# Optimization experiments

Hardware: AMD Instinct MI355X
Metric: run time of the kernel (lower is better)

Reference implementation:

```python
import jax, jax.numpy as jnp
import numpy as np

B, S, D, H, L = 16, 1024, 128, 8, 3
DFF = 4 * D  # 512
DH = D // H  # 16
NUM_CLASSES = 6


def layernorm(x, g, b, eps):
    mu = jnp.mean(x, axis=-1, keepdims=True)
    var = jnp.mean(jnp.square(x - mu), axis=-1, keepdims=True)
    return g * (x - mu) / jnp.sqrt(var + eps) + b


def setup_inputs() -> dict:
    key = jax.random.key(0)
    ks = jax.random.split(key, 16)
    sc = 0.05
    inp = {
        'x': jax.random.normal(ks[0], (B, S, D), dtype=jnp.float32),
        'Wq': jax.random.normal(ks[1], (L, D, D), dtype=jnp.float32) * sc,
        'bq': jnp.zeros((L, D), dtype=jnp.float32),
        'Wk': jax.random.normal(ks[2], (L, D, D), dtype=jnp.float32) * sc,
        'bk': jnp.zeros((L, D), dtype=jnp.float32),
        'Wv': jax.random.normal(ks[3], (L, D, D), dtype=jnp.float32) * sc,
        'bv': jnp.zeros((L, D), dtype=jnp.float32),
        'ln1_g': jnp.ones((L, D), dtype=jnp.float32),
        'ln1_b': jnp.zeros((L, D), dtype=jnp.float32),
        'W1': jax.random.normal(ks[4], (L, D, DFF), dtype=jnp.float32) * sc,
        'b1': jnp.zeros((L, DFF), dtype=jnp.float32),
        'W2': jax.random.normal(ks[5], (L, DFF, D), dtype=jnp.float32) * sc,
        'b2': jnp.zeros((L, D), dtype=jnp.float32),
        'ln2_g': jnp.ones((L, D), dtype=jnp.float32),
        'ln2_b': jnp.zeros((L, D), dtype=jnp.float32),
        'Wout': jax.random.normal(ks[6], (D, NUM_CLASSES), dtype=jnp.float32) * sc,
        'bout': jnp.zeros((NUM_CLASSES,), dtype=jnp.float32),
    }
    return inp


def reference(x, Wq, bq, Wk, bk, Wv, bv, ln1_g, ln1_b, W1, b1, W2, b2, ln2_g, ln2_b, Wout, bout):
    scale = 1.0 / jnp.sqrt(jnp.float32(DH))
    for l in range(L):
        # Q/K/V projections with ReLU activation (as in source Dense(..., relu))
        q = jax.nn.relu(jnp.einsum('bsd,de->bse', x, Wq[l]) + bq[l])
        k = jax.nn.relu(jnp.einsum('bsd,de->bse', x, Wk[l]) + bk[l])
        v = jax.nn.relu(jnp.einsum('bsd,de->bse', x, Wv[l]) + bv[l])
        # split-heads (tf.split axis=-1 / concat axis=0 == reshape to heads)
        qh = q.reshape(B, S, H, DH)
        kh = k.reshape(B, S, H, DH)
        vh = v.reshape(B, S, H, DH)
        scores = jnp.einsum('bqhd,bkhd->bhqk', qh, kh) * scale  # [B,H,S,S]
        attn = jax.nn.softmax(scores, axis=-1)
        o = jnp.einsum('bhqk,bkhd->bqhd', attn, vh).reshape(B, S, D)
        x = layernorm(o + x, ln1_g[l], ln1_b[l], 1e-8)
        # pointwise FFN (Conv1D kernel_size=1 == dense over last dim)
        h = jax.nn.relu(jnp.einsum('bsd,df->bsf', x, W1[l]) + b1[l])
        f = jnp.einsum('bsf,fd->bsd', h, W2[l]) + b2[l]
        x = layernorm(f + x, ln2_g[l], ln2_b[l], 1e-6)
    return jnp.einsum('bsd,dc->bsc', x, Wout) + bout
```

## Files before the change

kernel.cpp:

```cpp
#include <hip/hip_runtime.h>
#include <math.h>

#define Bq 16
#define Sq 1024
#define Dq 128
#define Hq 8
#define DHq 16
#define DFFq 512
#define Lq 3
#define NCLS 6
#define NROWS (Bq * Sq)
#define NX ((size_t)NROWS * Dq)

#define QSCL 0.36067376022224085f

typedef __attribute__((ext_vector_type(8))) short    bf16x8;
typedef __attribute__((ext_vector_type(4))) float    f32x4;
typedef __attribute__((ext_vector_type(4))) _Float16 f16x4;
typedef __attribute__((ext_vector_type(8))) _Float16 f16x8;
typedef __attribute__((ext_vector_type(2))) _Float16 f16x2;

__device__ inline ushort f32_to_bf16(float f) {
    union { float f; unsigned u; } v; v.f = f;
    unsigned r = v.u + 0x7fffu + ((v.u >> 16) & 1u);
    return (ushort)(r >> 16);
}

__device__ __forceinline__ float exp2_raw(float x) {
    float r;
    asm("v_exp_f32 %0, %1" : "=v"(r) : "v"(x));
    return r;
}

__device__ __forceinline__ float rcp_fast(float x) {
    float r;
    asm("v_rcp_f32 %0, %1" : "=v"(r) : "v"(x));
    return r;
}

__device__ __forceinline__ f16x2 pkrtz(float a, float b) {
    return __builtin_bit_cast(f16x2, __builtin_amdgcn_cvt_pkrtz(a, b));
}

__global__ __launch_bounds__(256) void prep_kernel(
    const float* __restrict__ Wqp, const float* __restrict__ Wkp,
    const float* __restrict__ Wvp, const float* __restrict__ W1p,
    const float* __restrict__ W2p, const float* __restrict__ xp,
    ushort* __restrict__ wbf, ushort* __restrict__ xbf)
{
    const int gid = blockIdx.x * 256 + threadIdx.x;
    if (gid < 147456) {
        const int w   = gid / 49152;
        const int rem = gid - w * 49152;
        const int l   = rem >> 14;
        const int idx = rem & 16383;
        const int k   = idx >> 7;
        const int n   = idx & 127;
        const float* src = (w == 0) ? Wqp : (w == 1) ? Wkp : Wvp;
        const float scl = (w == 0) ? QSCL : 1.0f;
        wbf[(size_t)(w * 3 + l) * 16384 + n * 128 + k] =
            f32_to_bf16(src[(size_t)l * 16384 + k * 128 + n] * scl);
    } else if (gid < 344064) {
        const int g   = gid - 147456;
        const int l   = g >> 16;
        const int idx = g & 65535;
        const int k   = idx >> 9;
        const int n   = idx & 511;
        wbf[147456 + (size_t)l * 65536 + n * 128 + k] =
            f32_to_bf16(W1p[(size_t)l * 65536 + k * 512 + n]);
    } else if (gid < 540672) {
        const int g   = gid - 344064;
        const int l   = g >> 16;
        const int idx = g & 65535;
        const int k   = idx >> 7;
        const int n   = idx & 127;
        wbf[344064 + (size_t)l * 65536 + n * 512 + k] =
            f32_to_bf16(W2p[(size_t)l * 65536 + k * 128 + n]);
    } else {
        const int g = gid - 540672;
        xbf[g] = f32_to_bf16(xp[g]);
    }
}

__global__ __launch_bounds__(256) void gemm_qkv(
    const ushort* __restrict__ A,
    const ushort* __restrict__ wq, const ushort* __restrict__ wk,
    const ushort* __restrict__ wv,
    const float* __restrict__ bqp, const float* __restrict__ bkp,
    const float* __restrict__ bvp,
    _Float16* __restrict__ qo, _Float16* __restrict__ ko,
    _Float16* __restrict__ vo)
{
    __shared__ ushort As[64 * 40];
    __shared__ ushort Bs[128 * 40];

    const int sel  = blockIdx.y;
    const ushort* Bt   = (sel == 0) ? wq : (sel == 1) ? wk : wv;
    const float*  bias = (sel == 0) ? bqp : (sel == 1) ? bkp : bvp;
    const float   bscl = (sel == 0) ? QSCL : 1.0f;

    const int tid  = threadIdx.x;
    const int row0 = blockIdx.x * 64;
    const int wave = tid >> 6;
    const int lane = tid & 63;
    const int quad = lane >> 4;
    const int m16  = lane & 15;
    const int wm   = wave >> 1;
    const int wn   = wave & 1;

    const int sar = tid >> 2;
    const int sac = (tid & 3) * 8;

    f32x4 acc[2][4];
    #pragma unroll
    for (int i = 0; i < 2; ++i)
        #pragma unroll
        for (int j = 0; j < 4; ++j) acc[i][j] = (f32x4)0.f;

    const int r1 = tid >> 2, r2 = r1 + 64;

    bf16x8 av  = *(const bf16x8*)(A  + (size_t)(row0 + sar) * 128 + sac);
    bf16x8 bv1 = *(const bf16x8*)(Bt + (size_t)r1 * 128 + sac);
    bf16x8 bv2 = *(const bf16x8*)(Bt + (size_t)r2 * 128 + sac);

    for (int k0 = 0; k0 < 128; k0 += 32) {
        __syncthreads();
        *(bf16x8*)&As[sar * 40 + sac] = av;
        *(bf16x8*)&Bs[r1 * 40 + sac]  = bv1;
        *(bf16x8*)&Bs[r2 * 40 + sac]  = bv2;
        __syncthreads();

        if (k0 < 96) {
            av  = *(const bf16x8*)(A  + (size_t)(row0 + sar) * 128 + k0 + 32 + sac);
            bv1 = *(const bf16x8*)(Bt + (size_t)r1 * 128 + k0 + 32 + sac);
            bv2 = *(const bf16x8*)(Bt + (size_t)r2 * 128 + k0 + 32 + sac);
        }

        bf16x8 af[2], bf[4];
        #pragma unroll
        for (int i = 0; i < 2; ++i)
            af[i] = *(const bf16x8*)&As[(32 * wm + 16 * i + m16) * 40 + quad * 8];
        #pragma unroll
        for (int j = 0; j < 4; ++j)
            bf[j] = *(const bf16x8*)&Bs[(64 * wn + 16 * j + m16) * 40 + quad * 8];
        #pragma unroll
        for (int i = 0; i < 2; ++i)
            #pragma unroll
            for (int j = 0; j < 4; ++j)
                acc[i][j] = __builtin_amdgcn_mfma_f32_16x16x32_bf16(af[i], bf[j], acc[i][j], 0, 0, 0);
    }

    #pragma unroll
    for (int i = 0; i < 2; ++i) {
        #pragma unroll
        for (int j = 0; j < 4; ++j) {
            const int col = 64 * wn + 16 * j + m16;
            const float bb = bias[col] * bscl;
            const int hh = col >> 4, dh = col & 15;
            #pragma unroll
            for (int r = 0; r < 4; ++r) {
                float val = fmaxf(acc[i][j][r] + bb, 0.f);
                const int gr = row0 + 32 * wm + 16 * i + quad * 4 + r;
                const int b = gr >> 10, s = gr & 1023;
                if (sel == 2) {
                    vo[(((size_t)b * Hq + hh) * DHq + dh) * Sq + s] = (_Float16)val;
                } else {
                    _Float16* outp = (sel == 0) ? qo : ko;
                    outp[(((size_t)b * Hq + hh) * Sq + s) * DHq + dh] = (_Float16)val;
                }
            }
        }
    }
}

__global__ __launch_bounds__(256, 3) void gemm_ffn_fused(
    const _Float16* __restrict__ o, const float* __restrict__ resid,
    const float* __restrict__ g1, const float* __restrict__ beta1,
    const ushort* __restrict__ W1t, const float* __restrict__ bias1,
    const ushort* __restrict__ W2t, const float* __restrict__ bias2,
    const float* __restrict__ g2, const float* __restrict__ beta2,
    float* __restrict__ xb,
    const ushort* __restrict__ wqn, const ushort* __restrict__ wkn,
    const ushort* __restrict__ wvn,
    const float* __restrict__ bqn, const float* __restrict__ bkn,
    const float* __restrict__ bvn,
    _Float16* __restrict__ qo, _Float16* __restrict__ ko,
    _Float16* __restrict__ vo, int do_next,
    const float* __restrict__ Wout, const float* __restrict__ bout,
    float* __restrict__ out, int last)
{
    __shared__ __align__(16) char smem[44544];
    ushort*    Af   = (ushort*)smem;
    ushort*    Hcc  = (ushort*)(smem + 8704);
    ushort*    Bs   = (ushort*)(smem + 17408);
    float*     wo_s = (float*)(smem + 17408);
    _Float16*  vals = (_Float16*)(smem + 35840);
    float*     mus  = (float*)(smem + 44288);
    float*     rsds = (float*)(smem + 44416);

    const int tid  = threadIdx.x;
    const int row0 = blockIdx.x * 32;
    const int wave = tid >> 6;
    const int lane = tid & 63;
    const int quad = lane >> 4;
    const int m16  = lane & 15;
    const int wm   = wave >> 1;
    const int wn   = wave & 1;
    const int sac  = (tid & 3) * 8;
    const int r1   = tid >> 2, r2 = r1 + 64;

    const int ca = lane * 2;
    const float2 gg  = *(const float2*)(g1 + ca);
    const float2 bt1 = *(const float2*)(beta1 + ca);
    f16x2  ovv[8];
    float2 rvv[8];
    #pragma unroll
    for (int it = 0; it < 8; ++it) {
        const size_t base = (size_t)(row0 + wave * 8 + it) * Dq;
        ovv[it] = *(const f16x2*)(o + base + ca);
        rvv[it] = *(const float2*)(resid + base + ca);
    }
    #pragma unroll
    for (int it = 0; it < 8; ++it) {
        const int rr = wave * 8 + it;
        const float v0 = (float)ovv[it][0] + rvv[it].x;
        const float v1 = (float)ovv[it][1] + rvv[it].y;

        float s = v0 + v1;
        #pragma unroll
        for (int off = 32; off > 0; off >>= 1) s += __shfl_xor(s, off, 64);
        const float mu = s * (1.f / 128.f);
        const float d0 = v0 - mu, d1 = v1 - mu;
        float vs = d0 * d0 + d1 * d1;
        #pragma unroll
        for (int off = 32; off > 0; off >>= 1) vs += __shfl_xor(vs, off, 64);
        const float rstd = rsqrtf(vs * (1.f / 128.f) + 1e-8f);

        const float rv0 = gg.x * d0 * rstd + bt1.x;
        const float rv1 = gg.y * d1 * rstd + bt1.y;
        ushort2 ab; ab.x = f32_to_bf16(rv0); ab.y = f32_to_bf16(rv1);
        *(ushort2*)&Af[rr * 136 + ca] = ab;
        f16x2 vv; vv[0] = (_Float16)rv0; vv[1] = (_Float16)rv1;
        *(f16x2*)&vals[rr * 132 + ca] = vv;
    }

    f32x4 acc[4], acc2[4];
    #pragma unroll
    for (int j = 0; j < 4; ++j) { acc[j] = (f32x4)0.f; acc2[j] = (f32x4)0.f; }

    bf16x8 w11 = *(const bf16x8*)(W1t + (size_t)r1 * 128 + sac);
    bf16x8 w12 = *(const bf16x8*)(W1t + (size_t)r1 * 128 + 32 + sac);
    bf16x8 w21 = *(const bf16x8*)(W1t + (size_t)r2 * 128 + sac);
    bf16x8 w22 = *(const bf16x8*)(W1t + (size_t)r2 * 128 + 32 + sac);

    #pragma unroll
    for (int t = 0; t < 16; ++t) {
        const int cc   = t >> 2;
        const int ph   = (t >> 1) & 1;
        const int half = t & 1;

        __syncthreads();
        *(bf16x8*)&Bs[r1 * 72 + sac]      = w11;
        *(bf16x8*)&Bs[r1 * 72 + 32 + sac] = w12;
        *(bf16x8*)&Bs[r2 * 72 + sac]      = w21;
        *(bf16x8*)&Bs[r2 * 72 + 32 + sac] = w22;
        __syncthreads();

        if (t < 15) {
            const int tn  = t + 1;
            const int nc  = tn >> 2, np = (tn >> 1) & 1, nh = tn & 1;
            if (np == 0) {
                const ushort* p = W1t + (size_t)(nc * 128) * 128 + nh * 64;
                w11 = *(const bf16x8*)(p + (size_t)r1 * 128 + sac);
                w12 = *(const bf16x8*)(p + (size_t)r1 * 128 + 32 + sac);
                w21 = *(const bf16x8*)(p + (size_t)r2 * 128 + sac);
                w22 = *(const bf16x8*)(p + (size_t)r2 * 128 + 32 + sac);
            } else {
                const ushort* p = W2t + nc * 128 + nh * 64;
                w11 = *(const bf16x8*)(p + (size_t)r1 * 512 + sac);
                w12 = *(const bf16x8*)(p + (size_t)r1 * 512 + 32 + sac);
                w21 = *(const bf16x8*)(p + (size_t)r2 * 512 + sac);
                w22 = *(const bf16x8*)(p + (size_t)r2 * 512 + 32 + sac);
            }
        } else if (do_next) {
            w11 = *(const bf16x8*)(wqn + (size_t)r1 * 128 + sac);
            w12 = *(const bf16x8*)(wqn + (size_t)r1 * 128 + 32 + sac);
            w21 = *(const bf16x8*)(wqn + (size_t)r2 * 128 + sac);
            w22 = *(const bf16x8*)(wqn + (size_t)r2 * 128 + 32 + sac);
        }

        const ushort* Asrc = ph ? Hcc : Af;
        #pragma unroll
        for (int hh = 0; hh < 2; ++hh) {
            const int kk = half * 64 + hh * 32;
            const bf16x8 af = *(const bf16x8*)&Asrc[(16 * wm + m16) * 136 + kk + quad * 8];
            bf16x8 bf[4];
            #pragma unroll
            for (int j = 0; j < 4; ++j)
                bf[j] = *(const bf16x8*)&Bs[(64 * wn + 16 * j + m16) * 72 + hh * 32 + quad * 8];
            if (ph == 0) {
                #pragma unroll
                for (int j = 0; j < 4; ++j)
                    acc[j] = __builtin_amdgcn_mfma_f32_16x16x32_bf16(af, bf[j], acc[j], 0, 0, 0);
            } else {
                #pragma unroll
                for (int j = 0; j < 4; ++j)
                    acc2[j] = __builtin_amdgcn_mfma_f32_16x16x32_bf16(af, bf[j], acc2[j], 0, 0, 0);
            }
        }

        if (ph == 0 && half == 1) {
            #pragma unroll
            for (int j = 0; j < 4; ++j) {
                const int col_l = 64 * wn + 16 * j + m16;
                const float bb = bias1[cc * 128 + col_l];
                #pragma unroll
                for (int r = 0; r < 4; ++r) {
                    const int row = 16 * wm + quad * 4 + r;
                    Hcc[row * 136 + col_l] = f32_to_bf16(fmaxf(acc[j][r] + bb, 0.f));
                }
                acc[j] = (f32x4)0.f;
            }
        }
    }

    __syncthreads();

    float vreg[4][4];
    #pragma unroll
    for (int j = 0; j < 4; ++j) {
        const int col = 64 * wn + 16 * j + m16;
        const float bb = bias2[col];
        #pragma unroll
        for (int r = 0; r < 4; ++r) {
            const int row = 16 * wm + quad * 4 + r;
            float v = acc2[j][r] + bb + (float)vals[row * 132 + col];
            vreg[j][r] = v;
            vals[row * 132 + col] = (_Float16)v;
        }
    }
    if (last) {
        #pragma unroll
        for (int i = 0; i < 3; ++i) wo_s[tid + i * 256] = Wout[tid + i * 256];
    }
    __syncthreads();

    {
        const int row = tid >> 3;
        const int c0  = (tid & 7) * 16;
        float s = 0.f, s2 = 0.f;
        #pragma unroll
        for (int u = 0; u < 4; ++u) {
            const f16x4 xv = *(const f16x4*)&vals[row * 132 + c0 + u * 4];
            #pragma unroll
            for (int e = 0; e < 4; ++e) {
                const float x = (float)xv[e];
                s += x; s2 = fmaf(x, x, s2);
            }
        }
        s  += __shfl_xor(s, 1, 64);  s  += __shfl_xor(s, 2, 64);  s  += __shfl_xor(s, 4, 64);
        s2 += __shfl_xor(s2, 1, 64); s2 += __shfl_xor(s2, 2, 64); s2 += __shfl_xor(s2, 4, 64);
        if ((tid & 7) == 0) {
            const float mu  = s * (1.f / 128.f);
            const float var = s2 * (1.f / 128.f) - mu * mu;
            mus[row]  = mu;
            rsds[row] = rsqrtf(var + 1e-6f);
        }
    }
    __syncthreads();

    if (!last) {
        #pragma unroll
        for (int j = 0; j < 4; ++j) {
            const int col = 64 * wn + 16 * j + m16;
            #pragma unroll
            for (int r = 0; r < 4; ++r) {
                const int row = 16 * wm + quad * 4 + r;
                const float rn = g2[col] * (vreg[j][r] - mus[row]) * rsds[row] + beta2[col];
                xb[(size_t)(row0 + row) * Dq + col] = rn;
                Af[row * 136 + col] = f32_to_bf16(rn);
            }
        }

        if (do_next) {
            f32x4 qacc[4];
            #pragma unroll
            for (int st = 0; st < 6; ++st) {
                const int sel  = st >> 1;
                const int half = st & 1;
                if (half == 0) {
                    #pragma unroll
                    for (int j = 0; j < 4; ++j) qacc[j] = (f32x4)0.f;
                }

                __syncthreads();
                *(bf16x8*)&Bs[r1 * 72 + sac]      = w11;
                *(bf16x8*)&Bs[r1 * 72 + 32 + sac] = w12;
                *(bf16x8*)&Bs[r2 * 72 + sac]      = w21;
                *(bf16x8*)&Bs[r2 * 72 + 32 + sac] = w22;
                __syncthreads();

                if (st < 5) {
                    const int sel2 = (st + 1) >> 1;
                    const int k02  = ((st + 1) & 1) * 64;
                    const ushort* Bt2 = (sel2 == 0) ? wqn : (sel2 == 1) ? wkn : wvn;
                    w11 = *(const bf16x8*)(Bt2 + (size_t)r1 * 128 + k02 + sac);
                    w12 = *(const bf16x8*)(Bt2 + (size_t)r1 * 128 + k02 + 32 + sac);
                    w21 = *(const bf16x8*)(Bt2 + (size_t)r2 * 128 + k02 + sac);
                    w22 = *(const bf16x8*)(Bt2 + (size_t)r2 * 128 + k02 + 32 + sac);
                }

                const int k0 = half * 64;
                #pragma unroll
                for (int hh = 0; hh < 2; ++hh) {
                    const int kk = k0 + hh * 32;
                    const bf16x8 af = *(const bf16x8*)&Af[(16 * wm + m16) * 136 + kk + quad * 8];
                    bf16x8 bf[4];
                    #pragma unroll
                    for (int j = 0; j < 4; ++j)
                        bf[j] = *(const bf16x8*)&Bs[(64 * wn + 16 * j + m16) * 72 + hh * 32 + quad * 8];
                    #pragma unroll
                    for (int j = 0; j < 4; ++j)
                        qacc[j] = __builtin_amdgcn_mfma_f32_16x16x32_bf16(af, bf[j], qacc[j], 0, 0, 0);
                }

                if (half) {
                    const float* bias = (sel == 0) ? bqn : (sel == 1) ? bkn : bvn;
                    const float  bscl = (sel == 0) ? QSCL : 1.0f;
                    #pragma unroll
                    for (int j = 0; j < 4; ++j) {
                        const int col = 64 * wn + 16 * j + m16;
                        const float bb = bias[col] * bscl;
                        const int hh = col >> 4, dh = col & 15;
                        #pragma unroll
                        for (int r = 0; r < 4; ++r) {
                            float val = fmaxf(qacc[j][r] + bb, 0.f);
                            const int gr = row0 + 16 * wm + quad * 4 + r;
                            const int b = gr >> 10, s = gr & 1023;
                            if (sel == 2) {
                                vo[(((size_t)b * Hq + hh) * DHq + dh) * Sq + s] = (_Float16)val;
                            } else {
                                _Float16* outp = (sel == 0) ? qo : ko;
                                outp[(((size_t)b * Hq + hh) * Sq + s) * DHq + dh] = (_Float16)val;
                            }
                        }
                    }
                }
            }
        }
    } else {
        #pragma unroll
        for (int j = 0; j < 4; ++j) {
            const int col = 64 * wn + 16 * j + m16;
            #pragma unroll
            for (int r = 0; r < 4; ++r) {
                const int row = 16 * wm + quad * 4 + r;
                vals[row * 132 + col] =
                    (_Float16)(g2[col] * (vreg[j][r] - mus[row]) * rsds[row] + beta2[col]);
            }
        }
        __syncthreads();
        if (tid < 32 * NCLS) {
            const int row = tid / NCLS;
            const int c   = tid - row * NCLS;
            float a = bout[c];
            #pragma unroll 8
            for (int kk = 0; kk < Dq; ++kk)
                a = fmaf((float)vals[row * 132 + kk], wo_s[kk * NCLS + c], a);
            out[(size_t)(row0 + row) * NCLS + c] = a;
        }
    }
}

__global__ __launch_bounds__(256) void attn_mfma(
    const _Float16* __restrict__ q, const _Float16* __restrict__ k,
    const _Float16* __restrict__ vt, _Float16* __restrict__ o)
{
    __shared__ _Float16 Ks[256 * 20];
    __shared__ _Float16 Vs[16 * 264];

    const int bh   = blockIdx.x;
    const int qc   = blockIdx.y;
    const int b    = bh >> 3;
    const int h    = bh & 7;
    const int tid  = threadIdx.x;
    const int wave = tid >> 6;
    const int lane = tid & 63;
    const int quad = lane >> 4;
    const int m16  = lane & 15;
    const int q0   = qc * 128 + wave * 32;

    const f16x4 qf0 = *(const f16x4*)(q + (((size_t)bh * Sq) + q0 + m16) * DHq + quad * 4);
    const f16x4 qf1 = *(const f16x4*)(q + (((size_t)bh * Sq) + q0 + 16 + m16) * DHq + quad * 4);

    const _Float16* kg  = k  + (size_t)bh * Sq * DHq;
    const _Float16* vtg = vt + (size_t)bh * DHq * Sq;

    f32x4 oacc0 = (f32x4)0.f, oacc1 = (f32x4)0.f;
    f32x4 dacc0 = (f32x4)0.f, dacc1 = (f32x4)0.f;

    f16x4 onesf;
    onesf[0] = (_Float16)1.f; onesf[1] = (_Float16)1.f;
    onesf[2] = (_Float16)1.f; onesf[3] = (_Float16)1.f;

    const int krow = tid;
    const int vrow = tid >> 4;
    const int vcol = (tid & 15) * 16;

    f16x8 ka  = *(const f16x8*)(kg + (size_t)krow * DHq);
    f16x8 kb8 = *(const f16x8*)(kg + (size_t)krow * DHq + 8);
    f16x8 va  = *(const f16x8*)(vtg + (size_t)vrow * Sq + vcol);
    f16x8 vb  = *(const f16x8*)(vtg + (size_t)vrow * Sq + vcol + 8);

    for (int kb = 0; kb < 4; ++kb) {
        __syncthreads();
        *(f16x8*)&Ks[krow * 20 + 0] = ka;
        *(f16x8*)&Ks[krow * 20 + 8] = kb8;
        *(f16x8*)&Vs[vrow * 264 + vcol + 0] = va;
        *(f16x8*)&Vs[vrow * 264 + vcol + 8] = vb;
        __syncthreads();

        if (kb < 3) {
            const _Float16* kp = kg  + ((size_t)(kb + 1) * 256 + krow) * DHq;
            const _Float16* vp = vtg + (size_t)vrow * Sq + (kb + 1) * 256 + vcol;
            ka  = *(const f16x8*)(kp);
            kb8 = *(const f16x8*)(kp + 8);
            va  = *(const f16x8*)(vp);
            vb  = *(const f16x8*)(vp + 8);
        }

        __builtin_amdgcn_s_setprio(1);
        #pragma unroll 4
        for (int kt = 0; kt < 16; ++kt) {
            const f16x4 kf = *(const f16x4*)&Ks[(kt * 16 + m16) * 20 + quad * 4];
            const f16x4 vf = *(const f16x4*)&Vs[m16 * 264 + kt * 16 + quad * 4];

            f32x4 st0 = __builtin_amdgcn_mfma_f32_16x16x16f16(kf, qf0, (f32x4)0.f, 0, 0, 0);
            f32x4 st1 = __builtin_amdgcn_mfma_f32_16x16x16f16(kf, qf1, (f32x4)0.f, 0, 0, 0);

            const f16x2 a0 = pkrtz(exp2_raw(st0[0]), exp2_raw(st0[1]));
            const f16x2 a1 = pkrtz(exp2_raw(st0[2]), exp2_raw(st0[3]));
            const f16x2 b0 = pkrtz(exp2_raw(st1[0]), exp2_raw(st1[1]));
            const f16x2 b1 = pkrtz(exp2_raw(st1[2]), exp2_raw(st1[3]));

            const f16x4 pf0 = __builtin_shufflevector(a0, a1, 0, 1, 2, 3);
            const f16x4 pf1 = __builtin_shufflevector(b0, b1, 0, 1, 2, 3);

            oacc0 = __builtin_amdgcn_mfma_f32_16x16x16f16(pf0, vf, oacc0, 0, 0, 0);
            oacc1 = __builtin_amdgcn_mfma_f32_16x16x16f16(pf1, vf, oacc1, 0, 0, 0);
            dacc0 = __builtin_amdgcn_mfma_f32_16x16x16f16(pf0, onesf, dacc0, 0, 0, 0);
            dacc1 = __builtin_amdgcn_mfma_f32_16x16x16f16(pf1, onesf, dacc1, 0, 0, 0);
        }
        __builtin_amdgcn_s_setprio(0);
    }

    #pragma unroll
    for (int r = 0; r < 4; ++r) {
        const float i0 = rcp_fast(dacc0[r]);
        const float i1 = rcp_fast(dacc1[r]);
        o[((size_t)b * Sq + q0 + quad * 4 + r) * Dq + h * DHq + m16]      = (_Float16)(oacc0[r] * i0);
        o[((size_t)b * Sq + q0 + 16 + quad * 4 + r) * Dq + h * DHq + m16] = (_Float16)(oacc1[r] * i1);
    }
}

extern "C" void kernel_launch(void* const* d_in, const int* in_sizes, int n_in,
                              void* d_out, int out_size, void* d_ws, size_t ws_size,
                              hipStream_t stream)
{
    const float* x_in  = (const float*)d_in[0];
    const float* Wq    = (const float*)d_in[1];
    const float* bq    = (const float*)d_in[2];
    const float* Wk    = (const float*)d_in[3];
    const float* bk    = (const float*)d_in[4];
    const float* Wv    = (const float*)d_in[5];
    const float* bv    = (const float*)d_in[6];
    const float* ln1_g = (const float*)d_in[7];
    const float* ln1_b = (const float*)d_in[8];
    const float* W1    = (const float*)d_in[9];
    const float* b1    = (const float*)d_in[10];
    const float* W2    = (const float*)d_in[11];
    const float* b2    = (const float*)d_in[12];
    const float* ln2_g = (const float*)d_in[13];
    const float* ln2_b = (const float*)d_in[14];
    const float* Wout  = (const float*)d_in[15];
    const float* bout  = (const float*)d_in[16];
    float* out = (float*)d_out;

    float* ws = (float*)d_ws;
    _Float16* qf16 = (_Float16*)ws;
    _Float16* kf16 = (_Float16*)(ws + NX / 2);
    _Float16* vt16 = (_Float16*)(ws + NX);
    float*    xb   = ws + 9 * NX / 2;
    ushort*   xbf0 = (ushort*)(ws + 11 * NX / 2);
    ushort*   wbf  = (ushort*)(ws + 7 * NX);
    _Float16* obuf = (_Float16*)(ws + 8 * NX);

    prep_kernel<<<dim3(10304), dim3(256), 0, stream>>>(Wq, Wk, Wv, W1, W2, x_in, wbf, xbf0);

    const dim3 blk(256);

    {
        const ushort* wqt = wbf + (size_t)0 * 16384;
        const ushort* wkt = wbf + (size_t)3 * 16384;
        const ushort* wvt = wbf + (size_t)6 * 16384;
        gemm_qkv<<<dim3(256, 3), blk, 0, stream>>>(
            xbf0, wqt, wkt, wvt, bq, bk, bv, qf16, kf16, vt16);
    }

    const float* xcur = x_in;
    for (int l = 0; l < Lq; ++l) {
        const ushort* w1t = wbf + 147456 + (size_t)l * 65536;
        const ushort* w2t = wbf + 344064 + (size_t)l * 65536;
        const int next = (l < Lq - 1) ? 1 : 0;
        const int ln   = l + 1;
        const ushort* wqn = next ? (wbf + (size_t)(0 * 3 + ln) * 16384) : wbf;
        const ushort* wkn = next ? (wbf + (size_t)(1 * 3 + ln) * 16384) : wbf;
        const ushort* wvn = next ? (wbf + (size_t)(2 * 3 + ln) * 16384) : wbf;
        const float*  bqn = next ? (bq + ln * Dq) : bq;
        const float*  bkn = next ? (bk + ln * Dq) : bk;
        const float*  bvn = next ? (bv + ln * Dq) : bv;

        attn_mfma<<<dim3(Bq * Hq, 8), blk, 0, stream>>>(qf16, kf16, vt16, obuf);

        gemm_ffn_fused<<<dim3(512), blk, 0, stream>>>(
            obuf, xcur, ln1_g + l * Dq, ln1_b + l * Dq,
            w1t, b1 + l * DFFq, w2t, b2 + l * Dq,
            ln2_g + l * Dq, ln2_b + l * Dq,
            xb,
            wqn, wkn, wvn, bqn, bkn, bvn,
            qf16, kf16, vt16, next,
            Wout, bout, out, (l == Lq - 1) ? 1 : 0);

        xcur = xb;
    }
}
```

Before: 240.7 us.

## Halve FFN block row tile to 16 rows and double grid size

Shrinks the fused FFN/LayerNorm/QKV kernel's row tile from 32 to 16 rows per block, giving each of the four waves a 16x32 output slice instead of a 2x2 wave grid, and launches 1024 blocks instead of 512. The aim is better fill of the GPU's compute units and lower per-block LDS, so more blocks can be resident. In exchange, every block still streams the full W1/W2/Wq/Wk/Wv weights, so weight traffic per row doubles and there are fewer MFMAs per weight load. It also adds a barrier before the next-layer QKV projection and drops the occupancy hint from the launch bounds.

```diff
diff --git a/kernel.cpp b/kernel.cpp
--- a/kernel.cpp
+++ b/kernel.cpp
@@ -173,7 +173,7 @@
     }
 }
 
-__global__ __launch_bounds__(256, 3) void gemm_ffn_fused(
+__global__ __launch_bounds__(256) void gemm_ffn_fused(
     const _Float16* __restrict__ o, const float* __restrict__ resid,
     const float* __restrict__ g1, const float* __restrict__ beta1,
     const ushort* __restrict__ W1t, const float* __restrict__ bias1,
@@ -189,40 +189,38 @@
     const float* __restrict__ Wout, const float* __restrict__ bout,
     float* __restrict__ out, int last)
 {
-    __shared__ __align__(16) char smem[44544];
+    __shared__ __align__(16) char smem[31488];
     ushort*    Af   = (ushort*)smem;
-    ushort*    Hcc  = (ushort*)(smem + 8704);
-    ushort*    Bs   = (ushort*)(smem + 17408);
-    float*     wo_s = (float*)(smem + 17408);
-    _Float16*  vals = (_Float16*)(smem + 35840);
-    float*     mus  = (float*)(smem + 44288);
-    float*     rsds = (float*)(smem + 44416);
+    ushort*    Hcc  = (ushort*)(smem + 4352);
+    ushort*    Bs   = (ushort*)(smem + 8704);
+    float*     wo_s = (float*)(smem + 8704);
+    _Float16*  vals = (_Float16*)(smem + 27136);
+    float*     mus  = (float*)(smem + 31360);
+    float*     rsds = (float*)(smem + 31424);
 
     const int tid  = threadIdx.x;
-    const int row0 = blockIdx.x * 32;
+    const int row0 = blockIdx.x * 16;
     const int wave = tid >> 6;
     const int lane = tid & 63;
     const int quad = lane >> 4;
     const int m16  = lane & 15;
-    const int wm   = wave >> 1;
-    const int wn   = wave & 1;
     const int sac  = (tid & 3) * 8;
     const int r1   = tid >> 2, r2 = r1 + 64;
 
     const int ca = lane * 2;
     const float2 gg  = *(const float2*)(g1 + ca);
     const float2 bt1 = *(const float2*)(beta1 + ca);
-    f16x2  ovv[8];
-    float2 rvv[8];
-    #pragma unroll
-    for (int it = 0; it < 8; ++it) {
-        const size_t base = (size_t)(row0 + wave * 8 + it) * Dq;
+    f16x2  ovv[4];
+    float2 rvv[4];
+    #pragma unroll
+    for (int it = 0; it < 4; ++it) {
+        const size_t base = (size_t)(row0 + wave * 4 + it) * Dq;
         ovv[it] = *(const f16x2*)(o + base + ca);
         rvv[it] = *(const float2*)(resid + base + ca);
     }
     #pragma unroll
-    for (int it = 0; it < 8; ++it) {
-        const int rr = wave * 8 + it;
+    for (int it = 0; it < 4; ++it) {
+        const int rr = wave * 4 + it;
         const float v0 = (float)ovv[it][0] + rvv[it].x;
         const float v1 = (float)ovv[it][1] + rvv[it].y;
 
@@ -244,9 +242,9 @@
         *(f16x2*)&vals[rr * 132 + ca] = vv;
     }
 
-    f32x4 acc[4], acc2[4];
-    #pragma unroll
-    for (int j = 0; j < 4; ++j) { acc[j] = (f32x4)0.f; acc2[j] = (f32x4)0.f; }
+    f32x4 acc[2], acc2[2];
+    #pragma unroll
+    for (int j = 0; j < 2; ++j) { acc[j] = (f32x4)0.f; acc2[j] = (f32x4)0.f; }
 
     bf16x8 w11 = *(const bf16x8*)(W1t + (size_t)r1 * 128 + sac);
     bf16x8 w12 = *(const bf16x8*)(W1t + (size_t)r1 * 128 + 32 + sac);
@@ -293,30 +291,30 @@
         #pragma unroll
         for (int hh = 0; hh < 2; ++hh) {
             const int kk = half * 64 + hh * 32;
-            const bf16x8 af = *(const bf16x8*)&Asrc[(16 * wm + m16) * 136 + kk + quad * 8];
-            bf16x8 bf[4];
-            #pragma unroll
-            for (int j = 0; j < 4; ++j)
-                bf[j] = *(const bf16x8*)&Bs[(64 * wn + 16 * j + m16) * 72 + hh * 32 + quad * 8];
+            const bf16x8 af = *(const bf16x8*)&Asrc[m16 * 136 + kk + quad * 8];
+            bf16x8 bf[2];
+            #pragma unroll
+            for (int j = 0; j < 2; ++j)
+                bf[j] = *(const bf16x8*)&Bs[(32 * wave + 16 * j + m16) * 72 + hh * 32 + quad * 8];
             if (ph == 0) {
                 #pragma unroll
-                for (int j = 0; j < 4; ++j)
+                for (int j = 0; j < 2; ++j)
                     acc[j] = __builtin_amdgcn_mfma_f32_16x16x32_bf16(af, bf[j], acc[j], 0, 0, 0);
             } else {
                 #pragma unroll
-                for (int j = 0; j < 4; ++j)
+                for (int j = 0; j < 2; ++j)
                     acc2[j] = __builtin_amdgcn_mfma_f32_16x16x32_bf16(af, bf[j], acc2[j], 0, 0, 0);
             }
         }
 
         if (ph == 0 && half == 1) {
             #pragma unroll
-            for (int j = 0; j < 4; ++j) {
-                const int col_l = 64 * wn + 16 * j + m16;
+            for (int j = 0; j < 2; ++j) {
+                const int col_l = 32 * wave + 16 * j + m16;
                 const float bb = bias1[cc * 128 + col_l];
                 #pragma unroll
                 for (int r = 0; r < 4; ++r) {
-                    const int row = 16 * wm + quad * 4 + r;
+                    const int row = quad * 4 + r;
                     Hcc[row * 136 + col_l] = f32_to_bf16(fmaxf(acc[j][r] + bb, 0.f));
                 }
                 acc[j] = (f32x4)0.f;
@@ -326,14 +324,14 @@
 
     __syncthreads();
 
-    float vreg[4][4];
-    #pragma unroll
-    for (int j = 0; j < 4; ++j) {
-        const int col = 64 * wn + 16 * j + m16;
+    float vreg[2][4];
+    #pragma unroll
+    for (int j = 0; j < 2; ++j) {
+        const int col = 32 * wave + 16 * j + m16;
         const float bb = bias2[col];
         #pragma unroll
         for (int r = 0; r < 4; ++r) {
-            const int row = 16 * wm + quad * 4 + r;
+            const int row = quad * 4 + r;
             float v = acc2[j][r] + bb + (float)vals[row * 132 + col];
             vreg[j][r] = v;
             vals[row * 132 + col] = (_Float16)v;
@@ -346,11 +344,11 @@
     __syncthreads();
 
     {
-        const int row = tid >> 3;
-        const int c0  = (tid & 7) * 16;
+        const int row = tid >> 4;
+        const int c0  = (tid & 15) * 8;
         float s = 0.f, s2 = 0.f;
         #pragma unroll
-        for (int u = 0; u < 4; ++u) {
+        for (int u = 0; u < 2; ++u) {
             const f16x4 xv = *(const f16x4*)&vals[row * 132 + c0 + u * 4];
             #pragma unroll
             for (int e = 0; e < 4; ++e) {
@@ -358,9 +356,11 @@
                 s += x; s2 = fmaf(x, x, s2);
             }
         }
-        s  += __shfl_xor(s, 1, 64);  s  += __shfl_xor(s, 2, 64);  s  += __shfl_xor(s, 4, 64);
-        s2 += __shfl_xor(s2, 1, 64); s2 += __shfl_xor(s2, 2, 64); s2 += __shfl_xor(s2, 4, 64);
-        if ((tid & 7) == 0) {
+        s  += __shfl_xor(s, 1, 64);  s  += __shfl_xor(s, 2, 64);
+        s  += __shfl_xor(s, 4, 64);  s  += __shfl_xor(s, 8, 64);
+        s2 += __shfl_xor(s2, 1, 64); s2 += __shfl_xor(s2, 2, 64);
+        s2 += __shfl_xor(s2, 4, 64); s2 += __shfl_xor(s2, 8, 64);
+        if ((tid & 15) == 0) {
             const float mu  = s * (1.f / 128.f);
             const float var = s2 * (1.f / 128.f) - mu * mu;
             mus[row]  = mu;
@@ -371,26 +371,27 @@
 
     if (!last) {
         #pragma unroll
-        for (int j = 0; j < 4; ++j) {
-            const int col = 64 * wn + 16 * j + m16;
+        for (int j = 0; j < 2; ++j) {
+            const int col = 32 * wave + 16 * j + m16;
             #pragma unroll
             for (int r = 0; r < 4; ++r) {
-                const int row = 16 * wm + quad * 4 + r;
+                const int row = quad * 4 + r;
                 const float rn = g2[col] * (vreg[j][r] - mus[row]) * rsds[row] + beta2[col];
                 xb[(size_t)(row0 + row) * Dq + col] = rn;
                 Af[row * 136 + col] = f32_to_bf16(rn);
             }
         }
+        __syncthreads();
 
         if (do_next) {
-            f32x4 qacc[4];
+            f32x4 qacc[2];
             #pragma unroll
             for (int st = 0; st < 6; ++st) {
                 const int sel  = st >> 1;
                 const int half = st & 1;
                 if (half == 0) {
                     #pragma unroll
-                    for (int j = 0; j < 4; ++j) qacc[j] = (f32x4)0.f;
+                    for (int j = 0; j < 2; ++j) qacc[j] = (f32x4)0.f;
                 }
 
                 __syncthreads();
@@ -414,13 +415,13 @@
                 #pragma unroll
                 for (int hh = 0; hh < 2; ++hh) {
                     const int kk = k0 + hh * 32;
-                    const bf16x8 af = *(const bf16x8*)&Af[(16 * wm + m16) * 136 + kk + quad * 8];
-                    bf16x8 bf[4];
+                    const bf16x8 af = *(const bf16x8*)&Af[m16 * 136 + kk + quad * 8];
+                    bf16x8 bf[2];
                     #pragma unroll
-                    for (int j = 0; j < 4; ++j)
-                        bf[j] = *(const bf16x8*)&Bs[(64 * wn + 16 * j + m16) * 72 + hh * 32 + quad * 8];
+                    for (int j = 0; j < 2; ++j)
+                        bf[j] = *(const bf16x8*)&Bs[(32 * wave + 16 * j + m16) * 72 + hh * 32 + quad * 8];
                     #pragma unroll
-                    for (int j = 0; j < 4; ++j)
+                    for (int j = 0; j < 2; ++j)
                         qacc[j] = __builtin_amdgcn_mfma_f32_16x16x32_bf16(af, bf[j], qacc[j], 0, 0, 0);
                 }
 
@@ -428,14 +429,14 @@
                     const float* bias = (sel == 0) ? bqn : (sel == 1) ? bkn : bvn;
                     const float  bscl = (sel == 0) ? QSCL : 1.0f;
                     #pragma unroll
-                    for (int j = 0; j < 4; ++j) {
-                        const int col = 64 * wn + 16 * j + m16;
+                    for (int j = 0; j < 2; ++j) {
+                        const int col = 32 * wave + 16 * j + m16;
                         const float bb = bias[col] * bscl;
                         const int hh = col >> 4, dh = col & 15;
                         #pragma unroll
                         for (int r = 0; r < 4; ++r) {
                             float val = fmaxf(qacc[j][r] + bb, 0.f);
-                            const int gr = row0 + 16 * wm + quad * 4 + r;
+                            const int gr = row0 + quad * 4 + r;
                             const int b = gr >> 10, s = gr & 1023;
                             if (sel == 2) {
                                 vo[(((size_t)b * Hq + hh) * DHq + dh) * Sq + s] = (_Float16)val;
@@ -450,17 +451,17 @@
         }
     } else {
         #pragma unroll
-        for (int j = 0; j < 4; ++j) {
-            const int col = 64 * wn + 16 * j + m16;
+        for (int j = 0; j < 2; ++j) {
+            const int col = 32 * wave + 16 * j + m16;
             #pragma unroll
             for (int r = 0; r < 4; ++r) {
-                const int row = 16 * wm + quad * 4 + r;
+                const int row = quad * 4 + r;
                 vals[row * 132 + col] =
                     (_Float16)(g2[col] * (vreg[j][r] - mus[row]) * rsds[row] + beta2[col]);
             }
         }
         __syncthreads();
-        if (tid < 32 * NCLS) {
+        if (tid < 16 * NCLS) {
             const int row = tid / NCLS;
             const int c   = tid - row * NCLS;
             float a = bout[c];
@@ -622,7 +623,7 @@
 
         attn_mfma<<<dim3(Bq * Hq, 8), blk, 0, stream>>>(qf16, kf16, vt16, obuf);
 
-        gemm_ffn_fused<<<dim3(512), blk, 0, stream>>>(
+        gemm_ffn_fused<<<dim3(1024), blk, 0, stream>>>(
             obuf, xcur, ln1_g + l * Dq, ln1_b + l * Dq,
             w1t, b1 + l * DFFq, w2t, b2 + l * Dq,
             ln2_g + l * Dq, ln2_b + l * Dq,
```

After: 251.5 us. +4.5%, slower.
